# Optimization experiments

Hardware: AMD Instinct MI355X
Metric: run time of the kernel (lower is better)

Reference implementation:

```python
import jax, jax.numpy as jnp
import numpy as np

V, D, H, F, L, SMAX = 32000, 768, 12, 3072, 6, 512
DN = D // H
NEG = -1e9
EPS = 1e-5


def _pos_encoding(S, d, dtype):
    # pe[pos,2i]   = sin(pos / 10000**(2i/d))
    # pe[pos,2i+1] = cos(pos / 10000**(2(i+1)/d))   (note the i+1, as in source)
    pos = jnp.arange(S, dtype=jnp.float32)[:, None]
    i = jnp.arange(d // 2, dtype=jnp.float32)[None, :]
    pe_sin = jnp.sin(pos / jnp.power(10000.0, 2.0 * i / d))
    pe_cos = jnp.cos(pos / jnp.power(10000.0, 2.0 * (i + 1.0) / d))
    pe = jnp.zeros((S, d), jnp.float32)
    pe = pe.at[:, 0::2].set(pe_sin).at[:, 1::2].set(pe_cos)
    return pe.astype(dtype)


def _layernorm(z, g, b):
    m = jnp.mean(z, axis=-1, keepdims=True)
    v = jnp.mean(jnp.square(z - m), axis=-1, keepdims=True)
    return (z - m) * jax.lax.rsqrt(v + EPS) * g + b


def setup_inputs() -> dict:
    key = jax.random.key(0)
    ks = jax.random.split(key, 20)
    s = 0.02
    inp = {
        "x": jax.random.randint(ks[0], (16, 512), 0, V, dtype=jnp.int64 if jax.config.read("jax_enable_x64") else jnp.int32),
        "padding_mask": jax.random.randint(ks[1], (16, 512, 512), 0, 2, dtype=jnp.int32),
        "emb": jax.random.normal(ks[2], (V, D), jnp.float32) * s,
        # per-head separate projections, stacked: [L, H, D, DN]
        "Wq": jax.random.normal(ks[3], (L, H, D, DN), jnp.float32) * s,
        "bq": jnp.zeros((L, H, DN), jnp.float32),
        "Wk": jax.random.normal(ks[4], (L, H, D, DN), jnp.float32) * s,
        "bk": jnp.zeros((L, H, DN), jnp.float32),
        "Wv": jax.random.normal(ks[5], (L, H, D, DN), jnp.float32) * s,
        "bv": jnp.zeros((L, H, DN), jnp.float32),
        "Wo": jax.random.normal(ks[6], (L, D, D), jnp.float32) * s,
        "bo": jnp.zeros((L, D), jnp.float32),
        "W1": jax.random.normal(ks[7], (L, D, F), jnp.float32) * s,
        "b1": jnp.zeros((L, F), jnp.float32),
        "W2": jax.random.normal(ks[8], (L, F, D), jnp.float32) * s,
        "b2": jnp.zeros((L, D), jnp.float32),
        "g1": jnp.ones((L, D), jnp.float32),
        "be1": jnp.zeros((L, D), jnp.float32),
        "g2": jnp.ones((L, D), jnp.float32),
        "be2": jnp.zeros((L, D), jnp.float32),
    }
    return inp


def reference(x, padding_mask, emb, Wq, bq, Wk, bk, Wv, bv, Wo, bo,
              W1, b1, W2, b2, g1, be1, g2, be2):
    B, S = x.shape
    h = emb[x]                                   # [B,S,D]
    h = h + _pos_encoding(S, D, h.dtype)[None]   # dropout is identity in eval
    bias = padding_mask.astype(h.dtype)[:, None] * NEG   # [B,1,S,S]
    scale = 1.0 / np.sqrt(DN)
    for l in range(L):
        q = jnp.einsum("bsd,hde->bhse", h, Wq[l]) + bq[l][None, :, None, :]
        k = jnp.einsum("bsd,hde->bhse", h, Wk[l]) + bk[l][None, :, None, :]
        v = jnp.einsum("bsd,hde->bhse", h, Wv[l]) + bv[l][None, :, None, :]
        scores = jnp.einsum("bhse,bhte->bhst", q, k) * scale + bias
        attn = jax.nn.softmax(scores, axis=-1)
        o = jnp.einsum("bhst,bhte->bhse", attn, v)        # [B,H,S,DN]
        o = o.transpose(0, 2, 1, 3).reshape(B, S, D)      # concat heads
        o = o @ Wo[l] + bo[l]
        h = _layernorm(h + o, g1[l], be1[l])
        ff = jax.nn.relu(h @ W1[l] + b1[l]) @ W2[l] + b2[l]
        h = _layernorm(h + ff, g2[l], be2[l])
    return h
```

## Files before the change

### kernel.cpp

```cpp
#include <hip/hip_runtime.h>
#include <hip/hip_bf16.h>
#include <math.h>

#define B_  16
#define S_  512
#define D_  768
#define H_  12
#define DN_ 64
#define F_  3072
#define L_  6
#define T_  (B_*S_)
#define QKVN 2304
#define TDC ((size_t)T_*D_)

typedef unsigned short ushort_t;
typedef short short8 __attribute__((ext_vector_type(8)));
typedef float floatx4 __attribute__((ext_vector_type(4)));

#define LDS_AS(p) ((__attribute__((address_space(3))) void*)(p))
#define GLB_AS(p) ((const __attribute__((address_space(1))) void*)(p))

static __device__ __forceinline__ float b2f(ushort_t u) {
  union { unsigned int i; float f; } x; x.i = ((unsigned int)u) << 16; return x.f;
}
static __device__ __forceinline__ ushort_t f2b(float f) {
  union { float f; unsigned int i; } x; x.f = f;
  unsigned int r = x.i + 0x7fffu + ((x.i >> 16) & 1u);
  return (ushort_t)(r >> 16);
}

__global__ __launch_bounds__(64) void probe_x(const int* __restrict__ x,
                                              int* __restrict__ xstride) {
  if (threadIdx.x == 0) {
    int allzero = 1;
    for (int i = 0; i < 64; ++i) allzero &= (x[2 * i + 1] == 0) ? 1 : 0;
    *xstride = allzero ? 2 : 1;
  }
}

__global__ __launch_bounds__(256) void pe_kernel(float* __restrict__ pe) {
  const int s = blockIdx.x;
  const float pos = (float)s;
  for (int d = threadIdx.x; d < D_; d += 256) {
    float v;
    if ((d & 1) == 0) {
      float freq = powf(10000.0f, -(float)d * (1.0f / 768.0f));
      v = sinf(pos * freq);
    } else {
      float freq = powf(10000.0f, -(float)(d + 1) * (1.0f / 768.0f));
      v = cosf(pos * freq);
    }
    pe[(size_t)s * D_ + d] = v;
  }
}

__global__ __launch_bounds__(256) void embed_pe(const int* __restrict__ x,
                                                const int* __restrict__ xstride,
                                                const float* __restrict__ emb,
                                                const float* __restrict__ pe,
                                                float* __restrict__ h32,
                                                ushort_t* __restrict__ h16) {
  const int t = blockIdx.x;
  const int s = t & (S_ - 1);
  const int tok = x[t * (*xstride)];
  const float* ep = emb + (size_t)tok * D_;
  const float* pp = pe + (size_t)s * D_;
  for (int d = threadIdx.x; d < D_; d += 256) {
    float v = ep[d] + pp[d];
    h32[(size_t)t * D_ + d] = v;
    h16[(size_t)t * D_ + d] = f2b(v);
  }
}

__global__ __launch_bounds__(256) void mask_bits(const int* __restrict__ mask,
                                                 unsigned long long* __restrict__ bits) {
  const int gw = (blockIdx.x * 256 + threadIdx.x) >> 6;
  const int lane = threadIdx.x & 63;
  const int m = mask[(size_t)gw * 64 + lane];
  unsigned long long bal = __ballot(m != 0);
  if (lane == 0) bits[gw] = bal;
}

__global__ __launch_bounds__(256) void pack_bias(const float* __restrict__ bq,
                                                 const float* __restrict__ bk,
                                                 const float* __restrict__ bv,
                                                 float* __restrict__ bqkv) {
  const int i = blockIdx.x * 256 + threadIdx.x;
  if (i < L_ * D_) {
    const int l = i / D_, c = i - l * D_;
    bqkv[(size_t)l * QKVN + c]          = bq[i];
    bqkv[(size_t)l * QKVN + 768 + c]    = bk[i];
    bqkv[(size_t)l * QKVN + 1536 + c]   = bv[i];
  }
}

__global__ __launch_bounds__(256) void transpose_cast(const float* __restrict__ in,
                                                      ushort_t* __restrict__ out,
                                                      int R, int C, int ZH,
                                                      size_t strideL, size_t strideH) {
  __shared__ float tb[32][33];
  const int c0 = blockIdx.x * 32, r0 = blockIdx.y * 32;
  const int z = blockIdx.z;
  const float* ib = in + (size_t)z * R * C;
  ushort_t* ob = out + (size_t)(z / ZH) * strideL + (size_t)(z % ZH) * strideH;
  const int i = threadIdx.x >> 5;
  const int j = threadIdx.x & 31;
  #pragma unroll
  for (int t = 0; t < 4; ++t)
    tb[i + 8 * t][j] = ib[(size_t)(r0 + i + 8 * t) * C + c0 + j];
  __syncthreads();
  #pragma unroll
  for (int t = 0; t < 4; ++t)
    ob[(size_t)(c0 + i + 8 * t) * R + r0 + j] = f2b(tb[j][i + 8 * t]);
}

__global__ __launch_bounds__(256) void transpose_v(const ushort_t* __restrict__ qkv,
                                                   ushort_t* __restrict__ vT) {
  __shared__ ushort_t tb[32][33];
  const int s0 = blockIdx.x * 32, e0 = blockIdx.y * 32;
  const int bh = blockIdx.z;
  const int b = bh / 12, hh = bh - b * 12;
  const int i = threadIdx.x >> 5, j = threadIdx.x & 31;
  #pragma unroll
  for (int t = 0; t < 4; ++t)
    tb[i + 8 * t][j] = qkv[((size_t)(b * S_ + s0 + i + 8 * t)) * QKVN + 1536 + hh * 64 + e0 + j];
  __syncthreads();
  #pragma unroll
  for (int t = 0; t < 4; ++t)
    vT[((size_t)(bh * 64 + e0 + i + 8 * t)) * S_ + s0 + j] = tb[j][i + 8 * t];
}

template<int RELU>
__global__ __launch_bounds__(256) void gemm_mfma(const ushort_t* __restrict__ A,
                                                 const ushort_t* __restrict__ Bt,
                                                 const float* __restrict__ bias,
                                                 ushort_t* __restrict__ C,
                                                 int N, int K) {
  __shared__ ushort_t Alds[128 * 32];
  __shared__ ushort_t Blds[128 * 32];
  const int tid = threadIdx.x;
  const int lane = tid & 63, wave = tid >> 6;
  const int l16 = lane & 15, quad = lane >> 4;
  const int m0 = (wave >> 1) * 64, n0 = (wave & 1) * 64;
  const int nb = gridDim.x;
  const int flat = blockIdx.y * nb + blockIdx.x;
  const int grp = flat / (8 * nb);
  const int rem = flat - grp * 8 * nb;
  const int bm = (grp * 8 + (rem & 7)) * 128;
  const int bn = (rem >> 3) * 128;
  const int r0 = tid >> 2, koff = (tid & 3) * 8;

  const ushort_t* ga0 = A  + (size_t)(bm + r0) * K + koff;
  const ushort_t* ga1 = ga0 + (size_t)64 * K;
  const ushort_t* gb0 = Bt + (size_t)(bn + r0) * K + koff;
  const ushort_t* gb1 = gb0 + (size_t)64 * K;
  ushort_t* la0 = &Alds[tid * 8];
  ushort_t* la1 = &Alds[64 * 32 + tid * 8];
  ushort_t* lb0 = &Blds[tid * 8];
  ushort_t* lb1 = &Blds[64 * 32 + tid * 8];

  floatx4 acc[4][4] = {};
  for (int k0 = 0; k0 < K; k0 += 32) {
    __syncthreads();
    __builtin_amdgcn_global_load_lds(GLB_AS(ga0 + k0), LDS_AS(la0), 16, 0, 0);
    __builtin_amdgcn_global_load_lds(GLB_AS(ga1 + k0), LDS_AS(la1), 16, 0, 0);
    __builtin_amdgcn_global_load_lds(GLB_AS(gb0 + k0), LDS_AS(lb0), 16, 0, 0);
    __builtin_amdgcn_global_load_lds(GLB_AS(gb1 + k0), LDS_AS(lb1), 16, 0, 0);
    __syncthreads();
    short8 af[4], bf[4];
    #pragma unroll
    for (int fi = 0; fi < 4; ++fi)
      af[fi] = *(const short8*)&Alds[(m0 + fi * 16 + l16) * 32 + quad * 8];
    #pragma unroll
    for (int fj = 0; fj < 4; ++fj)
      bf[fj] = *(const short8*)&Blds[(n0 + fj * 16 + l16) * 32 + quad * 8];
    #pragma unroll
    for (int fi = 0; fi < 4; ++fi)
      #pragma unroll
      for (int fj = 0; fj < 4; ++fj)
        acc[fi][fj] = __builtin_amdgcn_mfma_f32_16x16x32_bf16(af[fi], bf[fj], acc[fi][fj], 0, 0, 0);
  }
  #pragma unroll
  for (int fi = 0; fi < 4; ++fi) {
    #pragma unroll
    for (int fj = 0; fj < 4; ++fj) {
      const int row = bm + m0 + fi * 16 + quad * 4;
      const int col = bn + n0 + fj * 16 + l16;
      const float bv = bias[col];
      #pragma unroll
      for (int r = 0; r < 4; ++r) {
        float v = acc[fi][fj][r] + bv;
        if (RELU) v = fmaxf(v, 0.0f);
        C[(size_t)(row + r) * N + col] = f2b(v);
      }
    }
  }
}

__global__ __launch_bounds__(256) void gemm_mfma_sk(const ushort_t* __restrict__ A,
                                                    const ushort_t* __restrict__ Bt,
                                                    const float* __restrict__ bias,
                                                    ushort_t* __restrict__ P,
                                                    int N, int K) {
  __shared__ ushort_t Alds[128 * 32];
  __shared__ ushort_t Blds[128 * 32];
  const int tid = threadIdx.x;
  const int lane = tid & 63, wave = tid >> 6;
  const int l16 = lane & 15, quad = lane >> 4;
  const int m0 = (wave >> 1) * 64, n0 = (wave & 1) * 64;
  const int nb = gridDim.x;
  const int flat = blockIdx.y * nb + blockIdx.x;
  const int grp = flat / (8 * nb);
  const int rem = flat - grp * 8 * nb;
  const int bm = (grp * 8 + (rem & 7)) * 128;
  const int bn = (rem >> 3) * 128;
  const int r0 = tid >> 2, koff = (tid & 3) * 8;
  const int z = blockIdx.z;
  const int Kh = K >> 1;

  const ushort_t* ga0 = A  + (size_t)(bm + r0) * K + (size_t)z * Kh + koff;
  const ushort_t* ga1 = ga0 + (size_t)64 * K;
  const ushort_t* gb0 = Bt + (size_t)(bn + r0) * K + (size_t)z * Kh + koff;
  const ushort_t* gb1 = gb0 + (size_t)64 * K;
  ushort_t* la0 = &Alds[tid * 8];
  ushort_t* la1 = &Alds[64 * 32 + tid * 8];
  ushort_t* lb0 = &Blds[tid * 8];
  ushort_t* lb1 = &Blds[64 * 32 + tid * 8];
  ushort_t* Pz = P + (size_t)z * T_ * N;

  floatx4 acc[4][4] = {};
  for (int k0 = 0; k0 < Kh; k0 += 32) {
    __syncthreads();
    __builtin_amdgcn_global_load_lds(GLB_AS(ga0 + k0), LDS_AS(la0), 16, 0, 0);
    __builtin_amdgcn_global_load_lds(GLB_AS(ga1 + k0), LDS_AS(la1), 16, 0, 0);
    __builtin_amdgcn_global_load_lds(GLB_AS(gb0 + k0), LDS_AS(lb0), 16, 0, 0);
    __builtin_amdgcn_global_load_lds(GLB_AS(gb1 + k0), LDS_AS(lb1), 16, 0, 0);
    __syncthreads();
    short8 af[4], bf[4];
    #pragma unroll
    for (int fi = 0; fi < 4; ++fi)
      af[fi] = *(const short8*)&Alds[(m0 + fi * 16 + l16) * 32 + quad * 8];
    #pragma unroll
    for (int fj = 0; fj < 4; ++fj)
      bf[fj] = *(const short8*)&Blds[(n0 + fj * 16 + l16) * 32 + quad * 8];
    #pragma unroll
    for (int fi = 0; fi < 4; ++fi)
      #pragma unroll
      for (int fj = 0; fj < 4; ++fj)
        acc[fi][fj] = __builtin_amdgcn_mfma_f32_16x16x32_bf16(af[fi], bf[fj], acc[fi][fj], 0, 0, 0);
  }
  #pragma unroll
  for (int fi = 0; fi < 4; ++fi) {
    #pragma unroll
    for (int fj = 0; fj < 4; ++fj) {
      const int row = bm + m0 + fi * 16 + quad * 4;
      const int col = bn + n0 + fj * 16 + l16;
      const float bv = (z == 0) ? bias[col] : 0.0f;
      #pragma unroll
      for (int r = 0; r < 4; ++r) {
        float v = acc[fi][fj][r] + bv;
        Pz[(size_t)(row + r) * N + col] = f2b(v);
      }
    }
  }
}

__global__ __launch_bounds__(256) void attn_mfma(const ushort_t* __restrict__ qkv,
                                                 const ushort_t* __restrict__ vT,
                                                 const unsigned long long* __restrict__ mbits,
                                                 ushort_t* __restrict__ o) {
  __shared__ ushort_t Qs[64][72];
  __shared__ ushort_t Ks[64][72];
  __shared__ ushort_t Vt[64][72];
  __shared__ ushort_t Ps[64][72];
  const int F = blockIdx.x;
  const int xcd = F & 7;
  const int sfl = F >> 3;
  const int qt = sfl & 7;
  const int gg = sfl >> 3;
  const int bh = gg * 8 + xcd;
  const int b = bh / 12, hh = bh - b * 12;
  const int tid = threadIdx.x;
  const int lane = tid & 63, w = tid >> 6;
  const int l16 = lane & 15, quad = lane >> 4;

  for (int c = tid; c < 1024; c += 256) {
    const int row = c >> 4, e0 = (c & 15) * 4;
    *(ushort4*)&Qs[row][e0] =
        *(const ushort4*)(qkv + ((size_t)(b * S_ + qt * 64 + row)) * QKVN + hh * 64 + e0);
  }

  floatx4 Oa[4] = {};
  float mrow[4] = {-3e38f, -3e38f, -3e38f, -3e38f};
  float lrow[4] = {};
  const ushort_t* vbase = vT + ((size_t)(b * H_ + hh) * 64) * S_;

  for (int kt = 0; kt < 8; ++kt) {
    __syncthreads();
    for (int c = tid; c < 1024; c += 256) {
      const int row = c >> 4, e0 = (c & 15) * 4;
      *(ushort4*)&Ks[row][e0] =
          *(const ushort4*)(qkv + ((size_t)(b * S_ + kt * 64 + row)) * QKVN + 768 + hh * 64 + e0);
      *(ushort4*)&Vt[row][e0] =
          *(const ushort4*)(vbase + (size_t)row * S_ + kt * 64 + e0);
    }
    __syncthreads();

    floatx4 sa[4] = {};
    #pragma unroll
    for (int st = 0; st < 2; ++st) {
      short8 aq = *(const short8*)&Qs[w * 16 + l16][st * 32 + quad * 8];
      #pragma unroll
      for (int fj = 0; fj < 4; ++fj) {
        short8 bk = *(const short8*)&Ks[fj * 16 + l16][st * 32 + quad * 8];
        sa[fj] = __builtin_amdgcn_mfma_f32_16x16x32_bf16(aq, bk, sa[fj], 0, 0, 0);
      }
    }

    #pragma unroll
    for (int r = 0; r < 4; ++r) {
      const int qrow = qt * 64 + w * 16 + quad * 4 + r;
      const unsigned long long m64 = mbits[((size_t)(b * S_ + qrow) << 3) + kt];
      float s0 = sa[0][r] * 0.125f + (((m64 >> l16) & 1ull)        ? -1e9f : 0.0f);
      float s1 = sa[1][r] * 0.125f + (((m64 >> (16 + l16)) & 1ull) ? -1e9f : 0.0f);
      float s2 = sa[2][r] * 0.125f + (((m64 >> (32 + l16)) & 1ull) ? -1e9f : 0.0f);
      float s3 = sa[3][r] * 0.125f + (((m64 >> (48 + l16)) & 1ull) ? -1e9f : 0.0f);
      float mt = fmaxf(fmaxf(s0, s1), fmaxf(s2, s3));
      mt = fmaxf(mt, __shfl_xor(mt, 1)); mt = fmaxf(mt, __shfl_xor(mt, 2));
      mt = fmaxf(mt, __shfl_xor(mt, 4)); mt = fmaxf(mt, __shfl_xor(mt, 8));
      const float mn = fmaxf(mrow[r], mt);
      const float alpha = __expf(mrow[r] - mn);
      mrow[r] = mn;
      float p0 = __expf(s0 - mn), p1 = __expf(s1 - mn);
      float p2 = __expf(s2 - mn), p3 = __expf(s3 - mn);
      const int prow = w * 16 + quad * 4 + r;
      Ps[prow][ 0 + l16] = f2b(p0);
      Ps[prow][16 + l16] = f2b(p1);
      Ps[prow][32 + l16] = f2b(p2);
      Ps[prow][48 + l16] = f2b(p3);
      float rs = p0 + p1 + p2 + p3;
      rs += __shfl_xor(rs, 1); rs += __shfl_xor(rs, 2);
      rs += __shfl_xor(rs, 4); rs += __shfl_xor(rs, 8);
      lrow[r] = lrow[r] * alpha + rs;
      Oa[0][r] *= alpha; Oa[1][r] *= alpha; Oa[2][r] *= alpha; Oa[3][r] *= alpha;
    }

    #pragma unroll
    for (int st = 0; st < 2; ++st) {
      short8 ap = *(const short8*)&Ps[w * 16 + l16][st * 32 + quad * 8];
      #pragma unroll
      for (int fe = 0; fe < 4; ++fe) {
        short8 bv = *(const short8*)&Vt[fe * 16 + l16][st * 32 + quad * 8];
        Oa[fe] = __builtin_amdgcn_mfma_f32_16x16x32_bf16(ap, bv, Oa[fe], 0, 0, 0);
      }
    }
  }

  #pragma unroll
  for (int r = 0; r < 4; ++r) {
    const float inv = 1.0f / lrow[r];
    const size_t tok = (size_t)(b * S_ + qt * 64 + w * 16 + quad * 4 + r);
    #pragma unroll
    for (int fe = 0; fe < 4; ++fe)
      o[tok * D_ + hh * 64 + fe * 16 + l16] = f2b(Oa[fe][r] * inv);
  }
}

__global__ __launch_bounds__(256) void add_ln(float* __restrict__ h,
                                              const ushort_t* __restrict__ r,
                                              const float* __restrict__ g,
                                              const float* __restrict__ be,
                                              ushort_t* __restrict__ h16) {
  const int t = blockIdx.x;
  const int tid = threadIdx.x;
  __shared__ float red[8];
  const size_t base = (size_t)t * D_;
  float x0 = h[base + tid]       + b2f(r[base + tid])       + b2f(r[TDC + base + tid]);
  float x1 = h[base + tid + 256] + b2f(r[base + tid + 256]) + b2f(r[TDC + base + tid + 256]);
  float x2 = h[base + tid + 512] + b2f(r[base + tid + 512]) + b2f(r[TDC + base + tid + 512]);
  float s = x0 + x1 + x2;
  #pragma unroll
  for (int off = 32; off > 0; off >>= 1) s += __shfl_down(s, off);
  if ((tid & 63) == 0) red[tid >> 6] = s;
  __syncthreads();
  if (tid == 0) red[4] = (red[0] + red[1] + red[2] + red[3]) * (1.0f / 768.0f);
  __syncthreads();
  const float m = red[4];
  float d0 = x0 - m, d1 = x1 - m, d2 = x2 - m;
  float s2 = d0 * d0 + d1 * d1 + d2 * d2;
  #pragma unroll
  for (int off = 32; off > 0; off >>= 1) s2 += __shfl_down(s2, off);
  if ((tid & 63) == 0) red[tid >> 6] = s2;
  __syncthreads();
  if (tid == 0) red[5] = (red[0] + red[1] + red[2] + red[3]) * (1.0f / 768.0f);
  __syncthreads();
  const float rs = rsqrtf(red[5] + 1e-5f);
  float y0 = d0 * rs * g[tid]       + be[tid];
  float y1 = d1 * rs * g[tid + 256] + be[tid + 256];
  float y2 = d2 * rs * g[tid + 512] + be[tid + 512];
  h[base + tid]       = y0; h16[base + tid]       = f2b(y0);
  h[base + tid + 256] = y1; h16[base + tid + 256] = f2b(y1);
  h[base + tid + 512] = y2; h16[base + tid + 512] = f2b(y2);
}

__global__ __launch_bounds__(256) void write_out(const float* __restrict__ h,
                                                 float* __restrict__ out, int n) {
  int i = blockIdx.x * 256 + threadIdx.x;
  if (i < n) out[i] = h[i];
}

extern "C" void kernel_launch(void* const* d_in, const int* in_sizes, int n_in,
                              void* d_out, int out_size, void* d_ws, size_t ws_size,
                              hipStream_t stream) {
  (void)in_sizes; (void)n_in; (void)out_size; (void)ws_size;
  const int* x    = (const int*)d_in[0];
  const int* mask = (const int*)d_in[1];
  const float* emb = (const float*)d_in[2];
  const float* Wq  = (const float*)d_in[3];
  const float* bq  = (const float*)d_in[4];
  const float* Wk  = (const float*)d_in[5];
  const float* bk  = (const float*)d_in[6];
  const float* Wv  = (const float*)d_in[7];
  const float* bv  = (const float*)d_in[8];
  const float* Wo  = (const float*)d_in[9];
  const float* bo  = (const float*)d_in[10];
  const float* W1  = (const float*)d_in[11];
  const float* b1  = (const float*)d_in[12];
  const float* W2  = (const float*)d_in[13];
  const float* b2  = (const float*)d_in[14];
  const float* g1  = (const float*)d_in[15];
  const float* be1 = (const float*)d_in[16];
  const float* g2  = (const float*)d_in[17];
  const float* be2 = (const float*)d_in[18];

  const size_t TD  = TDC;
  const size_t DD  = (size_t)D_ * D_;
  const size_t WDD = (size_t)L_ * DD;
  const size_t WDF = (size_t)L_ * D_ * F_;

  float* h32 = (float*)d_ws;
  ushort_t* h16  = (ushort_t*)(h32 + TD);
  ushort_t* qkv16 = h16 + TD;
  ushort_t* o1   = qkv16 + 3 * TD;
  ushort_t* o2   = o1 + TD;
  ushort_t* ff   = qkv16;
  ushort_t* vT   = o2 + TD;
  ushort_t* bias16 = vT + TD;
  ushort_t* WqkvT = bias16 + (size_t)B_ * S_ * S_;
  ushort_t* WoT  = WqkvT + 3 * WDD;
  ushort_t* W1T  = WoT + WDD;
  ushort_t* W2T  = W1T + WDF;
  float* bqkv    = (float*)(W2T + WDF);
  int* xstride   = (int*)(bqkv + (size_t)L_ * QKVN);
  float* pe32    = (float*)o1;
  unsigned long long* mbits = (unsigned long long*)bias16;

  probe_x<<<dim3(1), 64, 0, stream>>>(x, xstride);
  pe_kernel<<<dim3(S_), 256, 0, stream>>>(pe32);
  transpose_cast<<<dim3(2, 24, 72), 256, 0, stream>>>(Wq, WqkvT,          768, 64, 12, 3 * DD, (size_t)64 * 768);
  transpose_cast<<<dim3(2, 24, 72), 256, 0, stream>>>(Wk, WqkvT + DD,     768, 64, 12, 3 * DD, (size_t)64 * 768);
  transpose_cast<<<dim3(2, 24, 72), 256, 0, stream>>>(Wv, WqkvT + 2 * DD, 768, 64, 12, 3 * DD, (size_t)64 * 768);
  transpose_cast<<<dim3(24, 24, 6), 256, 0, stream>>>(Wo, WoT, 768, 768, 1, DD, 0);
  transpose_cast<<<dim3(96, 24, 6), 256, 0, stream>>>(W1, W1T, 768, 3072, 1, (size_t)D_ * F_, 0);
  transpose_cast<<<dim3(24, 96, 6), 256, 0, stream>>>(W2, W2T, 3072, 768, 1, (size_t)D_ * F_, 0);
  pack_bias<<<dim3((L_ * D_ + 255) / 256), 256, 0, stream>>>(bq, bk, bv, bqkv);
  mask_bits<<<dim3((B_ * S_ * S_) / 256), 256, 0, stream>>>(mask, mbits);
  embed_pe<<<dim3(T_), 256, 0, stream>>>(x, xstride, emb, pe32, h32, h16);

  const dim3 gQKV(QKVN / 128, T_ / 128);
  const dim3 gDsk(D_ / 128, T_ / 128, 2);
  const dim3 gF(F_ / 128, T_ / 128);
  for (int l = 0; l < L_; ++l) {
    const size_t oDD = (size_t)l * DD;
    const size_t oDF = (size_t)l * D_ * F_;
    gemm_mfma<0><<<gQKV, 256, 0, stream>>>(h16, WqkvT + (size_t)l * 3 * DD, bqkv + (size_t)l * QKVN, qkv16, QKVN, D_);
    transpose_v<<<dim3(16, 2, B_ * H_), 256, 0, stream>>>(qkv16, vT);
    attn_mfma<<<dim3(8 * H_ * B_), 256, 0, stream>>>(qkv16, vT, mbits, o1);
    gemm_mfma_sk<<<gDsk, 256, 0, stream>>>(o1, WoT + oDD, bo + l * D_, o2, D_, D_);
    add_ln<<<dim3(T_), 256, 0, stream>>>(h32, o2, g1 + l * D_, be1 + l * D_, h16);
    gemm_mfma<1><<<gF, 256, 0, stream>>>(h16, W1T + oDF, b1 + l * F_, ff, F_, D_);
    gemm_mfma_sk<<<gDsk, 256, 0, stream>>>(ff, W2T + oDF, b2 + l * D_, o2, D_, F_);
    add_ln<<<dim3(T_), 256, 0, stream>>>(h32, o2, g2 + l * D_, be2 + l * D_, h16);
  }
  write_out<<<dim3((unsigned)(TD / 256)), 256, 0, stream>>>(h32, (float*)d_out, (int)TD);
}
```

Baseline: 1.987 ms.

## Double GEMM K-tile with XOR-swizzled LDS and register-prefetch K/V in attention

The two MFMA GEMM kernels now stage a 64-wide K slice per iteration instead of 32, halving the number of barrier pairs. They XOR-swizzle the LDS chunk layout on both the global-to-LDS load and the fragment reads to avoid bank conflicts. The attention kernel prefetches the next K and V tiles into registers while the current tile is processed. The costs are twice the LDS per block, which may lower occupancy, and more registers in attention.

Result: no change. 2.005 ms (+0.9%).

```diff
diff --git a/kernel.cpp b/kernel.cpp
--- a/kernel.cpp
+++ b/kernel.cpp
@@ -136,8 +136,8 @@
                                                  const float* __restrict__ bias,
                                                  ushort_t* __restrict__ C,
                                                  int N, int K) {
-  __shared__ ushort_t Alds[128 * 32];
-  __shared__ ushort_t Blds[128 * 32];
+  __shared__ ushort_t Alds[128 * 64];
+  __shared__ ushort_t Blds[128 * 64];
   const int tid = threadIdx.x;
   const int lane = tid & 63, wave = tid >> 6;
   const int l16 = lane & 15, quad = lane >> 4;
@@ -148,37 +148,44 @@
   const int rem = flat - grp * 8 * nb;
   const int bm = (grp * 8 + (rem & 7)) * 128;
   const int bn = (rem >> 3) * 128;
-  const int r0 = tid >> 2, koff = (tid & 3) * 8;
-
-  const ushort_t* ga0 = A  + (size_t)(bm + r0) * K + koff;
-  const ushort_t* ga1 = ga0 + (size_t)64 * K;
-  const ushort_t* gb0 = Bt + (size_t)(bn + r0) * K + koff;
-  const ushort_t* gb1 = gb0 + (size_t)64 * K;
-  ushort_t* la0 = &Alds[tid * 8];
-  ushort_t* la1 = &Alds[64 * 32 + tid * 8];
-  ushort_t* lb0 = &Blds[tid * 8];
-  ushort_t* lb1 = &Blds[64 * 32 + tid * 8];
+  const int r0 = tid >> 3;
+  const int ch = tid & 7;
+  const int koff = (ch ^ (r0 & 7)) * 8;
+
+  const ushort_t* ga = A  + (size_t)(bm + r0) * K + koff;
+  const ushort_t* gb = Bt + (size_t)(bn + r0) * K + koff;
+  ushort_t* la = &Alds[tid * 8];
+  ushort_t* lb = &Blds[tid * 8];
+  const int swz = l16 & 7;
 
   floatx4 acc[4][4] = {};
-  for (int k0 = 0; k0 < K; k0 += 32) {
+  for (int k0 = 0; k0 < K; k0 += 64) {
     __syncthreads();
-    __builtin_amdgcn_global_load_lds(GLB_AS(ga0 + k0), LDS_AS(la0), 16, 0, 0);
-    __builtin_amdgcn_global_load_lds(GLB_AS(ga1 + k0), LDS_AS(la1), 16, 0, 0);
-    __builtin_amdgcn_global_load_lds(GLB_AS(gb0 + k0), LDS_AS(lb0), 16, 0, 0);
-    __builtin_amdgcn_global_load_lds(GLB_AS(gb1 + k0), LDS_AS(lb1), 16, 0, 0);
+    #pragma unroll
+    for (int j = 0; j < 4; ++j) {
+      __builtin_amdgcn_global_load_lds(GLB_AS(ga + k0 + (size_t)(j * 32) * K), LDS_AS(la + j * 2048), 16, 0, 0);
+      __builtin_amdgcn_global_load_lds(GLB_AS(gb + k0 + (size_t)(j * 32) * K), LDS_AS(lb + j * 2048), 16, 0, 0);
+    }
     __syncthreads();
-    short8 af[4], bf[4];
-    #pragma unroll
-    for (int fi = 0; fi < 4; ++fi)
-      af[fi] = *(const short8*)&Alds[(m0 + fi * 16 + l16) * 32 + quad * 8];
-    #pragma unroll
-    for (int fj = 0; fj < 4; ++fj)
-      bf[fj] = *(const short8*)&Blds[(n0 + fj * 16 + l16) * 32 + quad * 8];
-    #pragma unroll
-    for (int fi = 0; fi < 4; ++fi)
-      #pragma unroll
-      for (int fj = 0; fj < 4; ++fj)
-        acc[fi][fj] = __builtin_amdgcn_mfma_f32_16x16x32_bf16(af[fi], bf[fj], acc[fi][fj], 0, 0, 0);
+    #pragma unroll
+    for (int kk = 0; kk < 2; ++kk) {
+      short8 af[4], bf[4];
+      #pragma unroll
+      for (int fi = 0; fi < 4; ++fi) {
+        const int row = m0 + fi * 16 + l16;
+        af[fi] = *(const short8*)&Alds[row * 64 + ((((kk << 2) + quad) ^ swz) * 8)];
+      }
+      #pragma unroll
+      for (int fj = 0; fj < 4; ++fj) {
+        const int row = n0 + fj * 16 + l16;
+        bf[fj] = *(const short8*)&Blds[row * 64 + ((((kk << 2) + quad) ^ swz) * 8)];
+      }
+      #pragma unroll
+      for (int fi = 0; fi < 4; ++fi)
+        #pragma unroll
+        for (int fj = 0; fj < 4; ++fj)
+          acc[fi][fj] = __builtin_amdgcn_mfma_f32_16x16x32_bf16(af[fi], bf[fj], acc[fi][fj], 0, 0, 0);
+    }
   }
   #pragma unroll
   for (int fi = 0; fi < 4; ++fi) {
@@ -202,8 +209,8 @@
                                                     const float* __restrict__ bias,
                                                     ushort_t* __restrict__ P,
                                                     int N, int K) {
-  __shared__ ushort_t Alds[128 * 32];
-  __shared__ ushort_t Blds[128 * 32];
+  __shared__ ushort_t Alds[128 * 64];
+  __shared__ ushort_t Blds[128 * 64];
   const int tid = threadIdx.x;
   const int lane = tid & 63, wave = tid >> 6;
   const int l16 = lane & 15, quad = lane >> 4;
@@ -214,40 +221,47 @@
   const int rem = flat - grp * 8 * nb;
   const int bm = (grp * 8 + (rem & 7)) * 128;
   const int bn = (rem >> 3) * 128;
-  const int r0 = tid >> 2, koff = (tid & 3) * 8;
+  const int r0 = tid >> 3;
+  const int ch = tid & 7;
+  const int koff = (ch ^ (r0 & 7)) * 8;
   const int z = blockIdx.z;
   const int Kh = K >> 1;
 
-  const ushort_t* ga0 = A  + (size_t)(bm + r0) * K + (size_t)z * Kh + koff;
-  const ushort_t* ga1 = ga0 + (size_t)64 * K;
-  const ushort_t* gb0 = Bt + (size_t)(bn + r0) * K + (size_t)z * Kh + koff;
-  const ushort_t* gb1 = gb0 + (size_t)64 * K;
-  ushort_t* la0 = &Alds[tid * 8];
-  ushort_t* la1 = &Alds[64 * 32 + tid * 8];
-  ushort_t* lb0 = &Blds[tid * 8];
-  ushort_t* lb1 = &Blds[64 * 32 + tid * 8];
+  const ushort_t* ga = A  + (size_t)(bm + r0) * K + (size_t)z * Kh + koff;
+  const ushort_t* gb = Bt + (size_t)(bn + r0) * K + (size_t)z * Kh + koff;
+  ushort_t* la = &Alds[tid * 8];
+  ushort_t* lb = &Blds[tid * 8];
   ushort_t* Pz = P + (size_t)z * T_ * N;
+  const int swz = l16 & 7;
 
   floatx4 acc[4][4] = {};
-  for (int k0 = 0; k0 < Kh; k0 += 32) {
+  for (int k0 = 0; k0 < Kh; k0 += 64) {
     __syncthreads();
-    __builtin_amdgcn_global_load_lds(GLB_AS(ga0 + k0), LDS_AS(la0), 16, 0, 0);
-    __builtin_amdgcn_global_load_lds(GLB_AS(ga1 + k0), LDS_AS(la1), 16, 0, 0);
-    __builtin_amdgcn_global_load_lds(GLB_AS(gb0 + k0), LDS_AS(lb0), 16, 0, 0);
-    __builtin_amdgcn_global_load_lds(GLB_AS(gb1 + k0), LDS_AS(lb1), 16, 0, 0);
+    #pragma unroll
+    for (int j = 0; j < 4; ++j) {
+      __builtin_amdgcn_global_load_lds(GLB_AS(ga + k0 + (size_t)(j * 32) * K), LDS_AS(la + j * 2048), 16, 0, 0);
+      __builtin_amdgcn_global_load_lds(GLB_AS(gb + k0 + (size_t)(j * 32) * K), LDS_AS(lb + j * 2048), 16, 0, 0);
+    }
     __syncthreads();
-    short8 af[4], bf[4];
-    #pragma unroll
-    for (int fi = 0; fi < 4; ++fi)
-      af[fi] = *(const short8*)&Alds[(m0 + fi * 16 + l16) * 32 + quad * 8];
-    #pragma unroll
-    for (int fj = 0; fj < 4; ++fj)
-      bf[fj] = *(const short8*)&Blds[(n0 + fj * 16 + l16) * 32 + quad * 8];
-    #pragma unroll
-    for (int fi = 0; fi < 4; ++fi)
-      #pragma unroll
-      for (int fj = 0; fj < 4; ++fj)
-        acc[fi][fj] = __builtin_amdgcn_mfma_f32_16x16x32_bf16(af[fi], bf[fj], acc[fi][fj], 0, 0, 0);
+    #pragma unroll
+    for (int kk = 0; kk < 2; ++kk) {
+      short8 af[4], bf[4];
+      #pragma unroll
+      for (int fi = 0; fi < 4; ++fi) {
+        const int row = m0 + fi * 16 + l16;
+        af[fi] = *(const short8*)&Alds[row * 64 + ((((kk << 2) + quad) ^ swz) * 8)];
+      }
+      #pragma unroll
+      for (int fj = 0; fj < 4; ++fj) {
+        const int row = n0 + fj * 16 + l16;
+        bf[fj] = *(const short8*)&Blds[row * 64 + ((((kk << 2) + quad) ^ swz) * 8)];
+      }
+      #pragma unroll
+      for (int fi = 0; fi < 4; ++fi)
+        #pragma unroll
+        for (int fj = 0; fj < 4; ++fj)
+          acc[fi][fj] = __builtin_amdgcn_mfma_f32_16x16x32_bf16(af[fi], bf[fj], acc[fi][fj], 0, 0, 0);
+    }
   }
   #pragma unroll
   for (int fi = 0; fi < 4; ++fi) {
@@ -295,14 +309,32 @@
   float lrow[4] = {};
   const ushort_t* vbase = vT + ((size_t)(b * H_ + hh) * 64) * S_;
 
+  ushort4 kreg[4], vreg[4];
+  #pragma unroll
+  for (int i = 0; i < 4; ++i) {
+    const int c = tid + i * 256;
+    const int row = c >> 4, e0 = (c & 15) * 4;
+    kreg[i] = *(const ushort4*)(qkv + ((size_t)(b * S_ + row)) * QKVN + 768 + hh * 64 + e0);
+    vreg[i] = *(const ushort4*)(vbase + (size_t)row * S_ + e0);
+  }
+
   for (int kt = 0; kt < 8; ++kt) {
     __syncthreads();
-    for (int c = tid; c < 1024; c += 256) {
+    #pragma unroll
+    for (int i = 0; i < 4; ++i) {
+      const int c = tid + i * 256;
       const int row = c >> 4, e0 = (c & 15) * 4;
-      *(ushort4*)&Ks[row][e0] =
-          *(const ushort4*)(qkv + ((size_t)(b * S_ + kt * 64 + row)) * QKVN + 768 + hh * 64 + e0);
-      *(ushort4*)&Vt[row][e0] =
-          *(const ushort4*)(vbase + (size_t)row * S_ + kt * 64 + e0);
+      *(ushort4*)&Ks[row][e0] = kreg[i];
+      *(ushort4*)&Vt[row][e0] = vreg[i];
+    }
+    if (kt < 7) {
+      #pragma unroll
+      for (int i = 0; i < 4; ++i) {
+        const int c = tid + i * 256;
+        const int row = c >> 4, e0 = (c & 15) * 4;
+        kreg[i] = *(const ushort4*)(qkv + ((size_t)(b * S_ + (kt + 1) * 64 + row)) * QKVN + 768 + hh * 64 + e0);
+        vreg[i] = *(const ushort4*)(vbase + (size_t)row * S_ + (kt + 1) * 64 + e0);
+      }
     }
     __syncthreads();
 
```
